# Performance work log

Hardware: AMD Instinct MI355X
Metric: run time of the kernel (lower is better)

## Reference

```python
import jax, jax.numpy as jnp
import numpy as np

B, S, E, H = 2, 2048, 4096, 32
D = E // H  # head_dim = 128
MAX_SEQ = 2048


def precompute_freqs(dim, end, theta=10000.0):
    # Faithful to the torch source, including its operator precedence:
    # freqs = 1.0 / (theta ** arange(0, dim, 2)[:dim//2].float() / dim)
    # i.e. 1.0 / ((theta ** exps) / dim); overflows to inf in fp32 -> freq 0.
    exps = jnp.arange(0, dim, 2, dtype=jnp.float32)[: dim // 2]
    freqs = 1.0 / (jnp.power(jnp.float32(theta), exps) / jnp.float32(dim))
    t = jnp.arange(end, dtype=jnp.float32)
    f = jnp.outer(t, freqs)  # [end, dim//2]
    return jnp.cos(f), jnp.sin(f)


def apply_rope(x, cos, sin, pos):
    # x: [B,H,S,D]; cos/sin: [max_seq, dim//2]; pos: [B,S]
    c = cos[pos][:, None]  # [B,1,S,f]
    s = sin[pos][:, None]
    xr = x.reshape(*x.shape[:-1], -1, 2)  # [B,H,S,D/2,2]
    x1, x2 = xr[..., 0], xr[..., 1]
    if x1.shape[-1] > c.shape[-1]:
        rep = x1.shape[-1] // c.shape[-1]  # repeat_interleave factor
        c = jnp.repeat(c, rep, axis=-1)
        s = jnp.repeat(s, rep, axis=-1)
    out = jnp.stack([x1 * c - x2 * s, x1 * s + x2 * c], axis=-1)
    return out.reshape(x.shape)


def setup_inputs() -> dict:
    key = jax.random.key(0)
    kx, kq, kk, kv, ko = jax.random.split(key, 5)
    x = jax.random.normal(kx, (B, S, E), jnp.float32)
    scale = 0.02
    Wq = jax.random.normal(kq, (E, E), jnp.float32) * scale
    Wk = jax.random.normal(kk, (E, E), jnp.float32) * scale
    Wv = jax.random.normal(kv, (E, E), jnp.float32) * scale
    Wo = jax.random.normal(ko, (E, E), jnp.float32) * scale
    z = jnp.zeros((E,), jnp.float32)
    return {"x": x, "Wq": Wq, "bq": z, "Wk": Wk, "bk": z, "Wv": Wv, "bv": z, "Wo": Wo, "bo": z}


def reference(x, Wq, bq, Wk, bk, Wv, bv, Wo, bo):
    cos, sin = precompute_freqs(H, MAX_SEQ)  # note: dim = n_heads, as in source
    pos = jnp.broadcast_to(jnp.arange(S)[None, :], (B, S))  # no offset, S <= max
    # QKV projections (torch Linear: x @ W.T + b)
    q = (x @ Wq.T + bq).reshape(B, S, H, D).transpose(0, 2, 1, 3)  # [B,H,S,D]
    k = (x @ Wk.T + bk).reshape(B, S, H, D).transpose(0, 2, 1, 3)
    v = (x @ Wv.T + bv).reshape(B, S, H, D).transpose(0, 2, 1, 3)
    q = apply_rope(q, cos, sin, pos)
    k = apply_rope(k, cos, sin, pos)
    # SDPA with mask=None (non-causal, full attention)
    scores = jnp.einsum("bhqd,bhkd->bhqk", q, k) / np.float32(np.sqrt(D))
    att = jax.nn.softmax(scores, axis=-1)
    out = jnp.einsum("bhqk,bhkd->bhqd", att, v)
    out = out.transpose(0, 2, 1, 3).reshape(B, S, E)
    return out @ Wo.T + bo
```

## Files before the change

kernel.cpp:

```cpp
#include <hip/hip_runtime.h>
#include <math.h>

typedef _Float16 half8 __attribute__((ext_vector_type(8)));
typedef _Float16 half4 __attribute__((ext_vector_type(4)));
typedef float f32x4 __attribute__((ext_vector_type(4)));

struct FreqT { float f[16]; };

__device__ __forceinline__ f32x4 mfma16(half8 a, half8 b, f32x4 c) {
  return __builtin_amdgcn_mfma_f32_16x16x32_f16(a, b, c, 0, 0, 0);
}

__device__ __forceinline__ void gload_lds16(const void* g, void* l) {
  __builtin_amdgcn_global_load_lds(
      (const __attribute__((address_space(1))) void*)g,
      (__attribute__((address_space(3))) void*)l, 16, 0, 0);
}

#define S_BARRIER() __builtin_amdgcn_s_barrier()
#define WAIT_LGKM0() asm volatile("s_waitcnt lgkmcnt(0)" ::: "memory")
#define WAIT_VM8() asm volatile("s_waitcnt vmcnt(8)" ::: "memory")
#define WAIT_VM4() asm volatile("s_waitcnt vmcnt(4)" ::: "memory")
#define WAIT_VM0() asm volatile("s_waitcnt vmcnt(0)" ::: "memory")

__global__ __launch_bounds__(256)
void cast_f32_f16(const float* __restrict__ in, _Float16* __restrict__ out, long n8) {
  long i = (long)blockIdx.x * blockDim.x + threadIdx.x;
  if (i >= n8) return;
  float4 a = ((const float4*)in)[2 * i];
  float4 b = ((const float4*)in)[2 * i + 1];
  half8 v;
  v[0] = (_Float16)a.x; v[1] = (_Float16)a.y; v[2] = (_Float16)a.z; v[3] = (_Float16)a.w;
  v[4] = (_Float16)b.x; v[5] = (_Float16)b.y; v[6] = (_Float16)b.z; v[7] = (_Float16)b.w;
  ((half8*)out)[i] = v;
}

#define GBM 256
#define GBN 256
#define GBK 64

template <typename OutT>
__global__ __launch_bounds__(512, 2)
void gemm256(const _Float16* __restrict__ A, const _Float16* __restrict__ W,
             const float* __restrict__ bias, OutT* __restrict__ C,
             int M, int N, int K) {
  __shared__ __align__(16) _Float16 lds[4][GBM * GBK];

  int nwg = gridDim.x;
  int bid = blockIdx.x;
  int cpx = nwg >> 3;
  int swz = (bid & 7) * cpx + (bid >> 3);
  int ntn = N / GBN;
  int m0 = (swz / ntn) * GBM, n0 = (swz % ntn) * GBN;

  int tid = threadIdx.x, lane = tid & 63, w = tid >> 6;
  int wm = w >> 2, wn = w & 3;
  int g = lane >> 4, lc = lane & 15;

  int r8 = w * 8 + (lane >> 3);
  int cs = (((lane & 7) ^ (lane >> 3)) << 3);
  const _Float16* gA = A + (size_t)(m0 + r8) * K + cs;
  const _Float16* gB = W + (size_t)(n0 + r8) * K + cs;

#define STAGE(bi, k0) do {                                            \
    _Float16* la_ = &lds[(bi) * 2][0] + w * 512;                      \
    _Float16* lb_ = &lds[(bi) * 2 + 1][0] + w * 512;                  \
    _Pragma("unroll")                                                 \
    for (int i_ = 0; i_ < 4; ++i_) {                                  \
      gload_lds16(gA + (size_t)(i_ * 64) * K + (k0), la_ + i_ * 4096);\
      gload_lds16(gB + (size_t)(i_ * 64) * K + (k0), lb_ + i_ * 4096);\
    } } while (0)

  int aOff[8], bOff[4];
#pragma unroll
  for (int mf = 0; mf < 8; ++mf) aOff[mf] = (wm * 128 + mf * 16 + lc) * 64;
#pragma unroll
  for (int nf = 0; nf < 4; ++nf) bOff[nf] = (wn * 64 + nf * 16 + lc) * 64;
  int co0 = (((0 * 4 + g) ^ (lc & 7)) << 3);
  int co1 = (((1 * 4 + g) ^ (lc & 7)) << 3);

  half8 a0[8], a1[8], b0[4], b1[4];
  f32x4 acc[8][4] = {};

#define LOAD_SET0(bi) do {                                            \
    const _Float16* lA_ = &lds[(bi) * 2][0];                          \
    const _Float16* lB_ = &lds[(bi) * 2 + 1][0];                      \
    _Pragma("unroll")                                                 \
    for (int mf = 0; mf < 4; ++mf) {                                  \
      a0[mf * 2 + 0] = *(const half8*)&lA_[aOff[mf] + co0];           \
      a0[mf * 2 + 1] = *(const half8*)&lA_[aOff[mf] + co1];           \
    }                                                                 \
    _Pragma("unroll")                                                 \
    for (int nf = 0; nf < 2; ++nf) {                                  \
      b0[nf * 2 + 0] = *(const half8*)&lB_[bOff[nf] + co0];           \
      b0[nf * 2 + 1] = *(const half8*)&lB_[bOff[nf] + co1];           \
    } } while (0)

#define LOAD_SET1(bi) do {                                            \
    const _Float16* lA_ = &lds[(bi) * 2][0];                          \
    const _Float16* lB_ = &lds[(bi) * 2 + 1][0];                      \
    _Pragma("unroll")                                                 \
    for (int mf = 0; mf < 4; ++mf) {                                  \
      a1[mf * 2 + 0] = *(const half8*)&lA_[aOff[mf + 4] + co0];       \
      a1[mf * 2 + 1] = *(const half8*)&lA_[aOff[mf + 4] + co1];       \
    }                                                                 \
    _Pragma("unroll")                                                 \
    for (int nf = 0; nf < 2; ++nf) {                                  \
      b1[nf * 2 + 0] = *(const half8*)&lB_[bOff[nf + 2] + co0];       \
      b1[nf * 2 + 1] = *(const half8*)&lB_[bOff[nf + 2] + co1];       \
    } } while (0)

#define MFMA_Q(mq, nq, ar, br) do {                                   \
    __builtin_amdgcn_s_setprio(1);                                    \
    _Pragma("unroll")                                                 \
    for (int mf = 0; mf < 4; ++mf)                                    \
      _Pragma("unroll")                                               \
      for (int nf = 0; nf < 2; ++nf)                                  \
        _Pragma("unroll")                                             \
        for (int kk = 0; kk < 2; ++kk)                                \
          acc[(mq) * 4 + mf][(nq) * 2 + nf] =                         \
              mfma16(ar[mf * 2 + kk], br[nf * 2 + kk],                \
                     acc[(mq) * 4 + mf][(nq) * 2 + nf]);              \
    __builtin_amdgcn_s_setprio(0); } while (0)

  const int NT = K >> 6;

  STAGE(0, 0);
  STAGE(1, GBK);
  WAIT_VM8();
  S_BARRIER();
  LOAD_SET0(0);

  for (int t = 0; t < NT - 2; ++t) {
    int cur = t & 1;
    LOAD_SET1(cur);
    MFMA_Q(0, 0, a0, b0);
    MFMA_Q(0, 1, a0, b1);
    WAIT_LGKM0();
    S_BARRIER();
    STAGE(cur, (t + 2) << 6);
    MFMA_Q(1, 1, a1, b1);
    MFMA_Q(1, 0, a1, b0);
    WAIT_VM8();
    S_BARRIER();
    LOAD_SET0(cur ^ 1);
  }
  {
    int cur = (NT - 2) & 1;
    LOAD_SET1(cur);
    MFMA_Q(0, 0, a0, b0);
    MFMA_Q(0, 1, a0, b1);
    MFMA_Q(1, 1, a1, b1);
    MFMA_Q(1, 0, a1, b0);
    WAIT_VM0();
    S_BARRIER();
    LOAD_SET0(cur ^ 1);
  }
  {
    LOAD_SET1((NT - 1) & 1);
    MFMA_Q(0, 0, a0, b0);
    MFMA_Q(0, 1, a0, b1);
    MFMA_Q(1, 1, a1, b1);
    MFMA_Q(1, 0, a1, b0);
  }

  int crow = m0 + wm * 128 + g * 4;
  int ccol = n0 + wn * 64 + lc;
#pragma unroll
  for (int nf = 0; nf < 4; ++nf) {
    float bv = bias[ccol + nf * 16];
#pragma unroll
    for (int mf = 0; mf < 8; ++mf)
#pragma unroll
      for (int j = 0; j < 4; ++j)
        C[(size_t)(crow + mf * 16 + j) * N + ccol + nf * 16] =
            (OutT)(acc[mf][nf][j] + bv);
  }
#undef STAGE
#undef LOAD_SET0
#undef LOAD_SET1
#undef MFMA_Q
}

__global__ __launch_bounds__(256)
void rope_kernel(_Float16* __restrict__ x, FreqT ft, int Sn, int E, long n8) {
  long i = (long)blockIdx.x * blockDim.x + threadIdx.x;
  if (i >= n8) return;
  int epr = E / 8;
  int e8 = (int)(i % epr);
  int s = (int)((i / epr) % Sn);
  int fj = e8 & 15;
  float fr = ft.f[fj];
  float ang = (float)s * fr;
  float sv, cv;
  sincosf(ang, &sv, &cv);
  half8 v = ((const half8*)x)[i];
  half8 o;
#pragma unroll
  for (int p = 0; p < 4; ++p) {
    float x1 = (float)v[2 * p], x2 = (float)v[2 * p + 1];
    o[2 * p] = (_Float16)(x1 * cv - x2 * sv);
    o[2 * p + 1] = (_Float16)(x1 * sv + x2 * cv);
  }
  ((half8*)x)[i] = o;
}

__global__ __launch_bounds__(256)
void transpose_v(const _Float16* __restrict__ v, _Float16* __restrict__ vt,
                 int Hn, int Sn) {
  const int D = 128;
  const int E = Hn * D;
  __shared__ _Float16 t[64][130];
  int spb = Sn / 64;
  int bid = blockIdx.x;
  int s0 = (bid % spb) * 64;
  int bh = bid / spb;
  int b = bh / Hn, h = bh % Hn;
  int tid = threadIdx.x;
  int r = tid >> 2, dc = (tid & 3) * 32;
  const _Float16* src = v + (size_t)(b * Sn + s0 + r) * E + h * D + dc;
#pragma unroll
  for (int i = 0; i < 4; ++i) {
    half8 x = *(const half8*)(src + i * 8);
#pragma unroll
    for (int k = 0; k < 4; ++k) {
      _Float16 a0 = x[2 * k], a1 = x[2 * k + 1];
      t[r][dc + i * 8 + 2 * k] = a0;
      t[r][dc + i * 8 + 2 * k + 1] = a1;
    }
  }
  __syncthreads();
  int d = tid >> 1, sh = (tid & 1) * 32;
  half8 ov[4];
#pragma unroll
  for (int c = 0; c < 4; ++c)
#pragma unroll
    for (int j = 0; j < 8; ++j)
      ov[c][j] = t[sh + c * 8 + j][d];
  _Float16* dst = vt + ((size_t)bh * D + d) * Sn + s0 + sh;
#pragma unroll
  for (int c = 0; c < 4; ++c)
    *(half8*)(dst + c * 8) = ov[c];
}

#define QB 128
#define KB 64

__global__ __launch_bounds__(256, 2)
void flash_attn(const _Float16* __restrict__ qg, const _Float16* __restrict__ kg,
                const _Float16* __restrict__ vt, _Float16* __restrict__ og,
                int Bn, int Hn, int Sn) {
  const int D = 128;
  const int E = Hn * D;

  __shared__ _Float16 Ksh[2][KB * 128];
  __shared__ _Float16 Vsh[D * KB];
  __shared__ _Float16 Psh[4][32 * 64];
  __shared__ float sm[4][32];

  int qtiles = Sn / QB;
  int bid = blockIdx.x;
  int bh = bid / qtiles, qt = bid % qtiles;
  int b = bh / Hn, h = bh % Hn;

  int tid = threadIdx.x, lane = tid & 63, w = tid >> 6;
  int g = lane >> 4, lc = lane & 15;
  int lc7 = lc & 7;

  const size_t headoff = ((size_t)b * Sn) * E + (size_t)h * D;
  const _Float16* qp = qg + headoff;
  const _Float16* kp = kg + headoff;
  const _Float16* vtp = vt + (size_t)(b * Hn + h) * D * Sn;

  int q0 = qt * QB + w * 32;
  half8 aq[2][4];
#pragma unroll
  for (int mf = 0; mf < 2; ++mf)
#pragma unroll
    for (int kf = 0; kf < 4; ++kf)
      aq[mf][kf] = *(const half8*)(qp + (size_t)(q0 + mf * 16 + lc) * E + kf * 32 + g * 8);

  float mrun[2] = {-1e30f, -1e30f}, lpart[2] = {0.f, 0.f};
  f32x4 o[2][8] = {};

  const float scale = 0.08838834764831845f;

  int krow = 4 * w + (lane >> 4);
  int kcol = ((lane & 15) ^ (krow & 7)) * 8;
  const _Float16* gK = kp + (size_t)krow * E + kcol;
  int vrow = w * 32 + (lane >> 3);
  int vcol = ((lane & 7) ^ (vrow & 7)) * 8;
  const _Float16* gV = vtp + (size_t)vrow * Sn + vcol;

  _Float16* Pw = Psh[w];
  float* smw = sm[w];

  const int NT = Sn / KB;

  {
    _Float16* lK = Ksh[0] + w * 512;
#pragma unroll
    for (int i = 0; i < 4; ++i)
      gload_lds16(gK + (size_t)(16 * i) * E, lK + i * 2048);
  }
  WAIT_VM0();
  S_BARRIER();

  for (int t = 0; t < NT; ++t) {
    int c = t & 1;
    {
      _Float16* lV = Vsh + w * 2048;
#pragma unroll
      for (int p = 0; p < 4; ++p)
        gload_lds16(gV + (size_t)(p * 8) * Sn + t * KB, lV + p * 512);
    }
    if (t + 1 < NT) {
      _Float16* lK = Ksh[c ^ 1] + w * 512;
#pragma unroll
      for (int i = 0; i < 4; ++i)
        gload_lds16(gK + (size_t)((t + 1) * KB + 16 * i) * E, lK + i * 2048);
    }

    f32x4 st[2][4] = {};
    {
      const _Float16* Kc = Ksh[c];
      __builtin_amdgcn_s_setprio(1);
#pragma unroll
      for (int kf = 0; kf < 4; ++kf) {
        half8 bk[4];
#pragma unroll
        for (int nf = 0; nf < 4; ++nf)
          bk[nf] = *(const half8*)&Kc[(nf * 16 + lc) * 128 + (((kf * 4 + g) ^ lc7) << 3)];
#pragma unroll
        for (int nf = 0; nf < 4; ++nf)
#pragma unroll
          for (int mf = 0; mf < 2; ++mf)
            st[mf][nf] = mfma16(bk[nf], aq[mf][kf], st[mf][nf]);
      }
      __builtin_amdgcn_s_setprio(0);
    }

    bool resc[2];
#pragma unroll
    for (int mf = 0; mf < 2; ++mf) {
      f32x4 m4 = st[mf][0];
#pragma unroll
      for (int nf = 1; nf < 4; ++nf)
#pragma unroll
        for (int j = 0; j < 4; ++j) m4[j] = fmaxf(m4[j], st[mf][nf][j]);
      float mx = fmaxf(fmaxf(m4[0], m4[1]), fmaxf(m4[2], m4[3]));
      mx = fmaxf(mx, __shfl_xor(mx, 16));
      mx = fmaxf(mx, __shfl_xor(mx, 32));
      mx *= scale;
      resc[mf] = __any(mx > mrun[mf] + 8.f);
      if (resc[mf]) {
        float mnew = fmaxf(mrun[mf], mx);
        float r = __expf(mrun[mf] - mnew);
        mrun[mf] = mnew;
        lpart[mf] *= r;
        if (g == 0) smw[mf * 16 + lc] = r;
      }
    }
#pragma unroll
    for (int mf = 0; mf < 2; ++mf)
      if (resc[mf]) {
        f32x4 rv = *(const f32x4*)&smw[mf * 16 + g * 4];
#pragma unroll
        for (int df = 0; df < 8; ++df)
#pragma unroll
          for (int j = 0; j < 4; ++j) o[mf][df][j] *= rv[j];
      }
#pragma unroll
    for (int mf = 0; mf < 2; ++mf) {
      int rowoff = (mf * 16 + lc) * 64;
#pragma unroll
      for (int nf = 0; nf < 4; ++nf) {
        half4 p4;
        float ls = 0.f;
#pragma unroll
        for (int j = 0; j < 4; ++j) {
          float p = __expf(st[mf][nf][j] * scale - mrun[mf]);
          ls += p;
          p4[j] = (_Float16)p;
        }
        lpart[mf] += ls;
        *(half4*)&Pw[rowoff + ((((nf * 2 + (g >> 1)) ^ lc7) << 3) + ((g & 1) << 2))] = p4;
      }
    }

    if (t + 1 < NT) { WAIT_VM4(); } else { WAIT_VM0(); }
    S_BARRIER();

    __builtin_amdgcn_s_setprio(1);
#pragma unroll
    for (int kk = 0; kk < 2; ++kk) {
      int csw = ((kk * 4 + g) ^ lc7) << 3;
      half8 ap0 = *(const half8*)&Pw[lc * 64 + csw];
      half8 ap1 = *(const half8*)&Pw[(16 + lc) * 64 + csw];
#pragma unroll
      for (int df = 0; df < 8; ++df) {
        half8 bv = *(const half8*)&Vsh[(df * 16 + lc) * 64 + csw];
        o[0][df] = mfma16(ap0, bv, o[0][df]);
        o[1][df] = mfma16(ap1, bv, o[1][df]);
      }
    }
    __builtin_amdgcn_s_setprio(0);

    if (t + 1 < NT) {
      WAIT_VM0();
      S_BARRIER();
    }
  }

#pragma unroll
  for (int mf = 0; mf < 2; ++mf) {
    float l = lpart[mf];
    l += __shfl_xor(l, 16);
    l += __shfl_xor(l, 32);
    if (g == 0) smw[mf * 16 + lc] = 1.0f / l;
  }
  _Float16* op = og + headoff;
#pragma unroll
  for (int mf = 0; mf < 2; ++mf) {
    f32x4 li = *(const f32x4*)&smw[mf * 16 + g * 4];
#pragma unroll
    for (int j = 0; j < 4; ++j) {
      int row = q0 + mf * 16 + g * 4 + j;
#pragma unroll
      for (int df = 0; df < 8; ++df)
        op[(size_t)row * E + df * 16 + lc] = (_Float16)(o[mf][df][j] * li[j]);
    }
  }
}

extern "C" void kernel_launch(void* const* d_in, const int* in_sizes, int n_in,
                              void* d_out, int out_size, void* d_ws, size_t ws_size,
                              hipStream_t stream) {
  const float* x  = (const float*)d_in[0];
  const float* Wq = (const float*)d_in[1];
  const float* bq = (const float*)d_in[2];
  const float* Wk = (const float*)d_in[3];
  const float* bk = (const float*)d_in[4];
  const float* Wv = (const float*)d_in[5];
  const float* bv = (const float*)d_in[6];
  const float* Wo = (const float*)d_in[7];
  const float* bo = (const float*)d_in[8];

  const int E = in_sizes[2];
  const int M = in_sizes[0] / E;
  const int S = 2048;
  const int Bb = M / S;
  const int H = 32;

  _Float16* xh = (_Float16*)d_ws;
  _Float16* wh = xh + (size_t)M * E;
  _Float16* qh = wh + (size_t)E * E;
  _Float16* kh = qh + (size_t)M * E;
  _Float16* vh = kh + (size_t)M * E;
  _Float16* oh = xh;
  _Float16* vtb = wh;

  FreqT ft;
  for (int j = 0; j < 16; ++j) {
    float pf = (float)pow(10000.0, (double)(2 * j));
    ft.f[j] = 1.0f / (pf / 32.0f);
  }

  long nx8 = (long)M * E / 8;
  long nw8 = (long)E * E / 8;
  dim3 blk(256);
  int cb_x = (int)((nx8 + 255) / 256);
  int cb_w = (int)((nw8 + 255) / 256);
  int gemm_grid = (M / GBM) * (E / GBN);

  cast_f32_f16<<<cb_x, blk, 0, stream>>>(x, xh, nx8);

  cast_f32_f16<<<cb_w, blk, 0, stream>>>(Wq, wh, nw8);
  gemm256<_Float16><<<gemm_grid, 512, 0, stream>>>(xh, wh, bq, qh, M, E, E);
  cast_f32_f16<<<cb_w, blk, 0, stream>>>(Wk, wh, nw8);
  gemm256<_Float16><<<gemm_grid, 512, 0, stream>>>(xh, wh, bk, kh, M, E, E);
  cast_f32_f16<<<cb_w, blk, 0, stream>>>(Wv, wh, nw8);
  gemm256<_Float16><<<gemm_grid, 512, 0, stream>>>(xh, wh, bv, vh, M, E, E);

  rope_kernel<<<cb_x, blk, 0, stream>>>(qh, ft, S, E, nx8);
  rope_kernel<<<cb_x, blk, 0, stream>>>(kh, ft, S, E, nx8);

  transpose_v<<<Bb * H * (S / 64), blk, 0, stream>>>(vh, vtb, H, S);

  flash_attn<<<Bb * H * (S / QB), blk, 0, stream>>>(qh, kh, vtb, oh, Bb, H, S);

  cast_f32_f16<<<cb_w, blk, 0, stream>>>(Wo, wh, nw8);
  gemm256<float><<<gemm_grid, 512, 0, stream>>>(oh, wh, bo, (float*)d_out, M, E, E);
}
```

Before: 772.0 us.

## Keep softmax P in registers via permlane swaps instead of LDS round trip

The softmax probabilities are packed to fp16 with cvt_pkrtz and rearranged into the MFMA A-operand layout using v_permlane32/16_swap, replacing the per-warp P write to shared memory and the read back. This removes LDS traffic and the Psh buffer, which frees LDS, and launch bounds are raised to 3 blocks per CU to try for higher occupancy. The risks are register pressure under the tighter launch bound and correctness of the lane permutation mapping. Rounding also changes from round-to-nearest to round-toward-zero.

```diff
diff --git a/kernel.cpp b/kernel.cpp
--- a/kernel.cpp
+++ b/kernel.cpp
@@ -3,6 +3,7 @@
 
 typedef _Float16 half8 __attribute__((ext_vector_type(8)));
 typedef _Float16 half4 __attribute__((ext_vector_type(4)));
+typedef __fp16 fp16x2 __attribute__((ext_vector_type(2)));
 typedef float f32x4 __attribute__((ext_vector_type(4)));
 
 struct FreqT { float f[16]; };
@@ -15,6 +16,12 @@
   __builtin_amdgcn_global_load_lds(
       (const __attribute__((address_space(1))) void*)g,
       (__attribute__((address_space(3))) void*)l, 16, 0, 0);
+}
+
+__device__ __forceinline__ unsigned pk_f16(float p0, float p1) {
+  union { fp16x2 h; unsigned u; } cvt;
+  cvt.h = __builtin_amdgcn_cvt_pkrtz(p0, p1);
+  return cvt.u;
 }
 
 #define S_BARRIER() __builtin_amdgcn_s_barrier()
@@ -246,7 +253,7 @@
 #define QB 128
 #define KB 64
 
-__global__ __launch_bounds__(256, 2)
+__global__ __launch_bounds__(256, 3)
 void flash_attn(const _Float16* __restrict__ qg, const _Float16* __restrict__ kg,
                 const _Float16* __restrict__ vt, _Float16* __restrict__ og,
                 int Bn, int Hn, int Sn) {
@@ -255,7 +262,6 @@
 
   __shared__ _Float16 Ksh[2][KB * 128];
   __shared__ _Float16 Vsh[D * KB];
-  __shared__ _Float16 Psh[4][32 * 64];
   __shared__ float sm[4][32];
 
   int qtiles = Sn / QB;
@@ -292,7 +298,6 @@
   int vcol = ((lane & 7) ^ (vrow & 7)) * 8;
   const _Float16* gV = vtp + (size_t)vrow * Sn + vcol;
 
-  _Float16* Pw = Psh[w];
   float* smw = sm[w];
 
   const int NT = Sn / KB;
@@ -370,22 +375,30 @@
 #pragma unroll
           for (int j = 0; j < 4; ++j) o[mf][df][j] *= rv[j];
       }
+
+    union PaU { unsigned u[4]; half8 h; } pa[2][2];
 #pragma unroll
     for (int mf = 0; mf < 2; ++mf) {
-      int rowoff = (mf * 16 + lc) * 64;
-#pragma unroll
-      for (int nf = 0; nf < 4; ++nf) {
-        half4 p4;
-        float ls = 0.f;
-#pragma unroll
-        for (int j = 0; j < 4; ++j) {
-          float p = __expf(st[mf][nf][j] * scale - mrun[mf]);
-          ls += p;
-          p4[j] = (_Float16)p;
+      unsigned pk[4][2];
+#pragma unroll
+      for (int nf = 0; nf < 4; ++nf)
+#pragma unroll
+        for (int jj = 0; jj < 2; ++jj) {
+          float p0 = __expf(st[mf][nf][2 * jj] * scale - mrun[mf]);
+          float p1 = __expf(st[mf][nf][2 * jj + 1] * scale - mrun[mf]);
+          lpart[mf] += p0 + p1;
+          pk[nf][jj] = pk_f16(p0, p1);
         }
-        lpart[mf] += ls;
-        *(half4*)&Pw[rowoff + ((((nf * 2 + (g >> 1)) ^ lc7) << 3) + ((g & 1) << 2))] = p4;
-      }
+#pragma unroll
+      for (int kk = 0; kk < 2; ++kk)
+#pragma unroll
+        for (int jj = 0; jj < 2; ++jj) {
+          unsigned A = pk[2 * kk][jj], B = pk[2 * kk + 1][jj];
+          asm volatile("v_permlane32_swap_b32 %0, %1" : "+v"(A), "+v"(B));
+          asm volatile("v_permlane16_swap_b32 %0, %1" : "+v"(A), "+v"(B));
+          pa[mf][kk].u[jj] = A;
+          pa[mf][kk].u[2 + jj] = B;
+        }
     }
 
     if (t + 1 < NT) { WAIT_VM4(); } else { WAIT_VM0(); }
@@ -395,13 +408,11 @@
 #pragma unroll
     for (int kk = 0; kk < 2; ++kk) {
       int csw = ((kk * 4 + g) ^ lc7) << 3;
-      half8 ap0 = *(const half8*)&Pw[lc * 64 + csw];
-      half8 ap1 = *(const half8*)&Pw[(16 + lc) * 64 + csw];
 #pragma unroll
       for (int df = 0; df < 8; ++df) {
         half8 bv = *(const half8*)&Vsh[(df * 16 + lc) * 64 + csw];
-        o[0][df] = mfma16(ap0, bv, o[0][df]);
-        o[1][df] = mfma16(ap1, bv, o[1][df]);
+        o[0][df] = mfma16(pa[0][kk].h, bv, o[0][df]);
+        o[1][df] = mfma16(pa[1][kk].h, bv, o[1][df]);
       }
     }
     __builtin_amdgcn_s_setprio(0);
```

After: 841.7 us. 9.0% more time.

## Keep softmax P in registers via permlane swaps instead of LDS round-trip

Applied to the files above, without the earlier changes.

Drops the per-wave P shared-memory buffer in the flash attention kernel. The exponentiated scores are packed into f16 pairs with cvt_pkrtz and rearranged across lanes with v_permlane32/16_swap so they land directly in MFMA A-operand layout. This removes the LDS writes and reads of P and frees LDS, which could help occupancy. In exchange it adds cross-lane permute instructions, switches to round-toward-zero conversion, and depends on getting the lane mapping exactly right.

```diff
diff --git a/kernel.cpp b/kernel.cpp
--- a/kernel.cpp
+++ b/kernel.cpp
@@ -3,7 +3,9 @@
 
 typedef _Float16 half8 __attribute__((ext_vector_type(8)));
 typedef _Float16 half4 __attribute__((ext_vector_type(4)));
+typedef __fp16 fp16x2 __attribute__((ext_vector_type(2)));
 typedef float f32x4 __attribute__((ext_vector_type(4)));
+typedef unsigned uint4v __attribute__((ext_vector_type(4)));
 
 struct FreqT { float f[16]; };
 
@@ -15,6 +17,11 @@
   __builtin_amdgcn_global_load_lds(
       (const __attribute__((address_space(1))) void*)g,
       (__attribute__((address_space(3))) void*)l, 16, 0, 0);
+}
+
+__device__ __forceinline__ unsigned pk_f16(float p0, float p1) {
+  fp16x2 h = __builtin_amdgcn_cvt_pkrtz(p0, p1);
+  return __builtin_bit_cast(unsigned, h);
 }
 
 #define S_BARRIER() __builtin_amdgcn_s_barrier()
@@ -255,7 +262,6 @@
 
   __shared__ _Float16 Ksh[2][KB * 128];
   __shared__ _Float16 Vsh[D * KB];
-  __shared__ _Float16 Psh[4][32 * 64];
   __shared__ float sm[4][32];
 
   int qtiles = Sn / QB;
@@ -292,7 +298,6 @@
   int vcol = ((lane & 7) ^ (vrow & 7)) * 8;
   const _Float16* gV = vtp + (size_t)vrow * Sn + vcol;
 
-  _Float16* Pw = Psh[w];
   float* smw = sm[w];
 
   const int NT = Sn / KB;
@@ -370,38 +375,70 @@
 #pragma unroll
           for (int j = 0; j < 4; ++j) o[mf][df][j] *= rv[j];
       }
-#pragma unroll
-    for (int mf = 0; mf < 2; ++mf) {
-      int rowoff = (mf * 16 + lc) * 64;
-#pragma unroll
-      for (int nf = 0; nf < 4; ++nf) {
-        half4 p4;
-        float ls = 0.f;
-#pragma unroll
-        for (int j = 0; j < 4; ++j) {
-          float p = __expf(st[mf][nf][j] * scale - mrun[mf]);
-          ls += p;
-          p4[j] = (_Float16)p;
-        }
-        lpart[mf] += ls;
-        *(half4*)&Pw[rowoff + ((((nf * 2 + (g >> 1)) ^ lc7) << 3) + ((g & 1) << 2))] = p4;
-      }
-    }
+
+    half8 pa00, pa01, pa10, pa11;
+#define PACK_P(MF, PA0, PA1) do {                                          \
+      float e0, e1;                                                        \
+      e0 = __expf(st[MF][0][0] * scale - mrun[MF]);                        \
+      e1 = __expf(st[MF][0][1] * scale - mrun[MF]);                        \
+      lpart[MF] += e0 + e1; unsigned k00 = pk_f16(e0, e1);                 \
+      e0 = __expf(st[MF][0][2] * scale - mrun[MF]);                        \
+      e1 = __expf(st[MF][0][3] * scale - mrun[MF]);                        \
+      lpart[MF] += e0 + e1; unsigned k01 = pk_f16(e0, e1);                 \
+      e0 = __expf(st[MF][1][0] * scale - mrun[MF]);                        \
+      e1 = __expf(st[MF][1][1] * scale - mrun[MF]);                        \
+      lpart[MF] += e0 + e1; unsigned k10 = pk_f16(e0, e1);                 \
+      e0 = __expf(st[MF][1][2] * scale - mrun[MF]);                        \
+      e1 = __expf(st[MF][1][3] * scale - mrun[MF]);                        \
+      lpart[MF] += e0 + e1; unsigned k11 = pk_f16(e0, e1);                 \
+      e0 = __expf(st[MF][2][0] * scale - mrun[MF]);                        \
+      e1 = __expf(st[MF][2][1] * scale - mrun[MF]);                        \
+      lpart[MF] += e0 + e1; unsigned k20 = pk_f16(e0, e1);                 \
+      e0 = __expf(st[MF][2][2] * scale - mrun[MF]);                        \
+      e1 = __expf(st[MF][2][3] * scale - mrun[MF]);                        \
+      lpart[MF] += e0 + e1; unsigned k21 = pk_f16(e0, e1);                 \
+      e0 = __expf(st[MF][3][0] * scale - mrun[MF]);                        \
+      e1 = __expf(st[MF][3][1] * scale - mrun[MF]);                        \
+      lpart[MF] += e0 + e1; unsigned k30 = pk_f16(e0, e1);                 \
+      e0 = __expf(st[MF][3][2] * scale - mrun[MF]);                        \
+      e1 = __expf(st[MF][3][3] * scale - mrun[MF]);                        \
+      lpart[MF] += e0 + e1; unsigned k31 = pk_f16(e0, e1);                 \
+      asm("v_permlane32_swap_b32 %0, %1" : "+v"(k00), "+v"(k10));          \
+      asm("v_permlane16_swap_b32 %0, %1" : "+v"(k00), "+v"(k10));          \
+      asm("v_permlane32_swap_b32 %0, %1" : "+v"(k01), "+v"(k11));          \
+      asm("v_permlane16_swap_b32 %0, %1" : "+v"(k01), "+v"(k11));          \
+      asm("v_permlane32_swap_b32 %0, %1" : "+v"(k20), "+v"(k30));          \
+      asm("v_permlane16_swap_b32 %0, %1" : "+v"(k20), "+v"(k30));          \
+      asm("v_permlane32_swap_b32 %0, %1" : "+v"(k21), "+v"(k31));          \
+      asm("v_permlane16_swap_b32 %0, %1" : "+v"(k21), "+v"(k31));          \
+      uint4v p0v, p1v;                                                     \
+      p0v[0] = k00; p0v[1] = k01; p0v[2] = k10; p0v[3] = k11;              \
+      p1v[0] = k20; p1v[1] = k21; p1v[2] = k30; p1v[3] = k31;              \
+      PA0 = __builtin_bit_cast(half8, p0v);                                \
+      PA1 = __builtin_bit_cast(half8, p1v);                                \
+    } while (0)
+    PACK_P(0, pa00, pa01);
+    PACK_P(1, pa10, pa11);
+#undef PACK_P
 
     if (t + 1 < NT) { WAIT_VM4(); } else { WAIT_VM0(); }
     S_BARRIER();
 
     __builtin_amdgcn_s_setprio(1);
-#pragma unroll
-    for (int kk = 0; kk < 2; ++kk) {
-      int csw = ((kk * 4 + g) ^ lc7) << 3;
-      half8 ap0 = *(const half8*)&Pw[lc * 64 + csw];
-      half8 ap1 = *(const half8*)&Pw[(16 + lc) * 64 + csw];
+    {
+      int csw0 = (g ^ lc7) << 3;
+      int csw1 = ((4 + g) ^ lc7) << 3;
 #pragma unroll
       for (int df = 0; df < 8; ++df) {
-        half8 bv = *(const half8*)&Vsh[(df * 16 + lc) * 64 + csw];
-        o[0][df] = mfma16(ap0, bv, o[0][df]);
-        o[1][df] = mfma16(ap1, bv, o[1][df]);
+        half8 bv0 = *(const half8*)&Vsh[(df * 16 + lc) * 64 + csw0];
+        o[0][df] = mfma16(pa00, bv0, o[0][df]);
+        o[1][df] = mfma16(pa10, bv0, o[1][df]);
+      }
+#pragma unroll
+      for (int df = 0; df < 8; ++df) {
+        half8 bv1 = *(const half8*)&Vsh[(df * 16 + lc) * 64 + csw1];
+        o[0][df] = mfma16(pa01, bv1, o[0][df]);
+        o[1][df] = mfma16(pa11, bv1, o[1][df]);
       }
     }
     __builtin_amdgcn_s_setprio(0);
```

Result: no change. 773.1 us (+0.1%).
